# Performance work log

Measured on AMD Instinct MI355X. Metric: run time of the kernel, lower is better.

Reference implementation:

```python
import jax, jax.numpy as jnp
import numpy as np

N = 100000   # nodes
H = 96       # hidden_dim
A = 32       # attn_dim
De = 16      # edge_embeddings_dim
E = 500000   # edges per edge type
NEG_SLOPE = 0.01  # torch F.leaky_relu default


def setup_inputs() -> dict:
    key = jax.random.key(0)
    ks = jax.random.split(key, 24)
    nrm = lambda k, shape, s=1.0: jax.random.normal(k, shape, dtype=jnp.float32) * s
    idx = lambda k: jax.random.randint(k, (E,), 0, N, dtype=jnp.int32)
    Din = 2 * H + De
    return {
        'h': nrm(ks[0], (N, H)),
        'src0': idx(ks[1]), 'dst0': idx(ks[2]),
        'src1': idx(ks[3]), 'dst1': idx(ks[4]),
        'src2': idx(ks[5]), 'dst2': idx(ks[6]),
        'Wm0': nrm(ks[7], (Din, H), Din ** -0.5), 'bm0': jnp.zeros((H,), jnp.float32), 'ef0': nrm(ks[8], (De,)),
        'Wm1': nrm(ks[9], (Din, H), Din ** -0.5), 'bm1': jnp.zeros((H,), jnp.float32), 'ef1': nrm(ks[10], (De,)),
        'Wm2': nrm(ks[11], (Din, H), Din ** -0.5), 'bm2': jnp.zeros((H,), jnp.float32), 'ef2': nrm(ks[12], (De,)),
        'Wn0': nrm(ks[13], (H, A), H ** -0.5), 'Wa0': nrm(ks[14], (2 * A, 1), (2 * A) ** -0.5),
        'Wn1': nrm(ks[15], (H, A), H ** -0.5), 'Wa1': nrm(ks[16], (2 * A, 1), (2 * A) ** -0.5),
        'Wu': nrm(ks[17], (4 * H, H), (4 * H) ** -0.5), 'bu': jnp.zeros((H,), jnp.float32),
    }


def _leaky(x):
    return jnp.where(x > 0, x, NEG_SLOPE * x)


def _edge_msg(h, src, dst, Wm, bm, ef):
    # cat(src_h, dst_h, edge_feature) -> Linear  (dropout p=0, eval mode)
    x = jnp.concatenate([h[src], h[dst], jnp.broadcast_to(ef, (src.shape[0], ef.shape[0]))], axis=-1)
    return x @ Wm + bm  # [E, H]


def _mean_agg(m, dst):
    # fn.mean('m','msg'): per-destination mean over incoming edges
    s = jax.ops.segment_sum(m, dst, num_segments=N)
    c = jax.ops.segment_sum(jnp.ones((m.shape[0],), m.dtype), dst, num_segments=N)
    return s / jnp.maximum(c, 1.0)[:, None]


def _attn_agg(scores, m, dst):
    # per-destination softmax over mailbox (variable-size), then weighted sum
    smax = jax.ops.segment_max(scores, dst, num_segments=N)
    ex = jnp.exp(scores - smax[dst])
    den = jax.ops.segment_sum(ex, dst, num_segments=N)
    num = jax.ops.segment_sum(ex[:, None] * m, dst, num_segments=N)
    return num / jnp.maximum(den, 1e-9)[:, None]


def reference(h, src0, dst0, src1, dst1, src2, dst2,
              Wm0, bm0, ef0, Wm1, bm1, ef1, Wm2, bm2, ef2,
              Wn0, Wa0, Wn1, Wa1, Wu, bu):
    # edge type 0: intra_diff (attention), type 1: inter_diff (attention), type 2: intra_lt (mean)
    m0 = _edge_msg(h, src0, dst0, Wm0, bm0, ef0)
    m1 = _edge_msg(h, src1, dst1, Wm1, bm1, ef1)
    m2 = _edge_msg(h, src2, dst2, Wm2, bm2, ef2)

    z0 = h @ Wn0  # [N, A]
    s0 = _leaky(jnp.concatenate([z0[src0], z0[dst0]], axis=-1) @ Wa0)[:, 0]  # [E]
    z1 = h @ Wn1
    s1 = _leaky(jnp.concatenate([z1[src1], z1[dst1]], axis=-1) @ Wa1)[:, 0]

    msg0 = _attn_agg(s0, m0, dst0)   # [N, H]
    msg1 = _attn_agg(s1, m1, dst1)
    msg2 = _mean_agg(m2, dst2)

    # cross_reducer='stack' then concat over edge-type dim -> [N, 3H]
    mcat = jnp.concatenate([msg0, msg1, msg2], axis=-1)
    # cell node update: Linear(cat(h, m)) + ReLU
    return jax.nn.relu(jnp.concatenate([h, mcat], axis=-1) @ Wu + bu)
```

## Files before the change

### kernel.cpp

```cpp
#include <hip/hip_runtime.h>
#include <hip/hip_bf16.h>
#include <cstdint>

#define NN 100000
#define HH 96
#define AD 32
#define DE 16
#define EE 500000
#define NEG 0.01f

#define GSH 10
#define GSZ 1024
#define KB 98
#define CH 4096
#define BPT 123

typedef __bf16 bf16x8 __attribute__((ext_vector_type(8)));
typedef float  f32x4  __attribute__((ext_vector_type(4)));

__device__ __forceinline__ unsigned short f2b(float x) {
    union { float f; unsigned int u; } v; v.f = x;
    unsigned int r = v.u + 0x7fffu + ((v.u >> 16) & 1u);
    return (unsigned short)(r >> 16);
}
__device__ __forceinline__ float b2f(unsigned short h) {
    union { unsigned int u; float f; } v; v.u = ((unsigned int)h) << 16;
    return v.f;
}

__global__ void prep_kernel(const float* Wm0, const float* bm0, const float* ef0,
                            const float* Wm1, const float* bm1, const float* ef1,
                            const float* Wm2, const float* bm2, const float* ef2,
                            const float* Wn0, const float* Wa0,
                            const float* Wn1, const float* Wa1,
                            const float* Wu,
                            float* cvec, float* wvec,
                            unsigned short* BfN, unsigned short* BfU) {
    const float* Wm[3] = {Wm0, Wm1, Wm2};
    const float* bm[3] = {bm0, bm1, bm2};
    const float* ef[3] = {ef0, ef1, ef2};
    const int total = 288 + 384 + 55296 + 36864;
    for (int i = blockIdx.x * blockDim.x + threadIdx.x; i < total;
         i += gridDim.x * blockDim.x) {
        if (i < 288) {
            int t = i / 96, j = i % 96;
            float s = bm[t][j];
            for (int k = 0; k < DE; ++k) s += ef[t][k] * Wm[t][(2 * HH + k) * HH + j];
            cvec[i] = s;
        } else if (i < 288 + 384) {
            int ii = i - 288;
            int kind = ii / 96, k = ii % 96;
            const float* Wn = (kind < 2) ? Wn0 : Wn1;
            const float* Wa = (kind < 2) ? Wa0 : Wa1;
            int off = (kind & 1) ? AD : 0;
            float s = 0.f;
            for (int a = 0; a < AD; ++a) s += Wn[k * AD + a] * Wa[off + a];
            wvec[ii] = s;
        } else if (i < 288 + 384 + 55296) {
            int ii = i - 672;
            int sec = ii / 9216; int rem = ii % 9216;
            int ksc = rem / 512; int lj = rem % 512;
            int ks = ksc / 6, c = ksc % 6;
            int lane = lj / 8, jj = lj % 8;
            int quad = lane / 16, m = lane % 16;
            int k = ks * 32 + quad * 8 + jj;
            int n = c * 16 + m;
            int mt = (sec < 3) ? sec : sec - 3;
            int rowoff = (sec < 3) ? 0 : HH;
            BfN[ii] = f2b(Wm[mt][(rowoff + k) * HH + n]);
        } else {
            int ii = i - (672 + 55296);
            int ksc = ii / 512; int lj = ii % 512;
            int ks = ksc / 6, c = ksc % 6;
            int lane = lj / 8, jj = lj % 8;
            int quad = lane / 16, m = lane % 16;
            int k = ks * 32 + quad * 8 + jj;
            int n = c * 16 + m;
            BfU[ii] = f2b(Wu[k * HH + n]);
        }
    }
}

__global__ void cast_uv_kernel(const float* __restrict__ h, const float* __restrict__ wvec,
                               unsigned short* __restrict__ hb, float* __restrict__ uv) {
    int lane = threadIdx.x & 31;
    int node = (blockIdx.x * blockDim.x + threadIdx.x) >> 5;
    if (node >= NN) return;
    float h0 = h[node * HH + lane];
    float h1 = h[node * HH + 32 + lane];
    float h2 = h[node * HH + 64 + lane];
    hb[node * HH + lane] = f2b(h0);
    hb[node * HH + 32 + lane] = f2b(h1);
    hb[node * HH + 64 + lane] = f2b(h2);
    float acc[4];
#pragma unroll
    for (int q = 0; q < 4; ++q)
        acc[q] = h0 * wvec[q * 96 + lane] + h1 * wvec[q * 96 + 32 + lane] +
                 h2 * wvec[q * 96 + 64 + lane];
#pragma unroll
    for (int d = 16; d >= 1; d >>= 1)
#pragma unroll
        for (int q = 0; q < 4; ++q) acc[q] += __shfl_down(acc[q], d, 32);
    if (lane == 0) {
#pragma unroll
        for (int q = 0; q < 4; ++q) uv[q * NN + node] = acc[q];
    }
}

__global__ void zero_kernel(float4* __restrict__ p, int n4) {
    for (int i = blockIdx.x * blockDim.x + threadIdx.x; i < n4;
         i += gridDim.x * blockDim.x)
        p[i] = make_float4(0.f, 0.f, 0.f, 0.f);
}

__global__ void bucket_hist(const int* __restrict__ d0, const int* __restrict__ d1,
                            const int* __restrict__ d2, int* __restrict__ bCnt) {
    __shared__ int hist[3 * KB];
    int t = threadIdx.x;
    for (int j = t; j < 3 * KB; j += 256) hist[j] = 0;
    __syncthreads();
    const int total = 3 * EE;
    for (int i = blockIdx.x * blockDim.x + t; i < total; i += gridDim.x * blockDim.x) {
        int ty = i / EE, e = i - ty * EE;
        const int* d = (ty == 0) ? d0 : (ty == 1) ? d1 : d2;
        atomicAdd(&hist[ty * KB + (d[e] >> GSH)], 1);
    }
    __syncthreads();
    for (int j = t; j < 3 * KB; j += 256)
        if (hist[j]) atomicAdd(&bCnt[j], hist[j]);
}

__global__ void bucket_scan(const int* __restrict__ bCnt, int* __restrict__ bBase,
                            int* __restrict__ gCursor, int* __restrict__ rs) {
    __shared__ int hist[3 * KB];
    int t = threadIdx.x;
    if (t < 3 * KB) hist[t] = bCnt[t];
    __syncthreads();
    if (t < 3) {
        int run = 0;
        for (int b = 0; b < KB; ++b) {
            bBase[t * (KB + 1) + b] = run;
            gCursor[t * KB + b] = run;
            run += hist[t * KB + b];
        }
        bBase[t * (KB + 1) + KB] = run;
        rs[(size_t)t * (NN + 1) + NN] = run;
    }
}

__global__ __launch_bounds__(256) void bucket_scatter(
    const int* __restrict__ s0, const int* __restrict__ d0,
    const int* __restrict__ s1, const int* __restrict__ d1,
    const int* __restrict__ s2, const int* __restrict__ d2,
    int* __restrict__ gCursor, unsigned int* __restrict__ binned) {
    __shared__ unsigned int recs[CH];
    __shared__ unsigned short rnk[CH];
    __shared__ unsigned char bkt[CH];
    __shared__ int cnt[KB];
    __shared__ int gpos[KB];
    int t = threadIdx.x;
    int type = blockIdx.x / BPT;
    int chunk = (blockIdx.x % BPT) * CH;
    const int* src = (type == 0) ? s0 : (type == 1) ? s1 : s2;
    const int* dst = (type == 0) ? d0 : (type == 1) ? d1 : d2;
    if (t < KB) cnt[t] = 0;
    __syncthreads();
#pragma unroll
    for (int k = 0; k < CH / 256; ++k) {
        int idx = k * 256 + t;
        int e = chunk + idx;
        if (e < EE) {
            int s = src[e], d = dst[e];
            int b = d >> GSH;
            recs[idx] = ((unsigned int)s << GSH) | (unsigned int)(d & (GSZ - 1));
            bkt[idx] = (unsigned char)b;
            rnk[idx] = (unsigned short)atomicAdd(&cnt[b], 1);
        } else {
            bkt[idx] = 0xFF;
        }
    }
    __syncthreads();
    if (t < KB) {
        int c = cnt[t];
        gpos[t] = (c > 0) ? atomicAdd(&gCursor[type * KB + t], c) : 0;
    }
    __syncthreads();
    unsigned int* bout = binned + (size_t)type * EE;
#pragma unroll
    for (int k = 0; k < CH / 256; ++k) {
        int idx = k * 256 + t;
        unsigned char b = bkt[idx];
        if (b != 0xFF) bout[gpos[b] + rnk[idx]] = recs[idx];
    }
}

__global__ __launch_bounds__(256) void bucket_sort(
    const unsigned int* __restrict__ binned, const int* __restrict__ bBase,
    int* __restrict__ rs, int* __restrict__ sorted) {
    __shared__ int cnt[GSZ];
    __shared__ int tsum[256];
    int t = threadIdx.x;
    int type = blockIdx.x / KB;
    int b = blockIdx.x % KB;
    int nodeBase = b * GSZ;
    int eb = bBase[type * (KB + 1) + b];
    int en = bBase[type * (KB + 1) + b + 1];
    int n = en - eb;
    const unsigned int* bin = binned + (size_t)type * EE + eb;
#pragma unroll
    for (int k = 0; k < GSZ / 256; ++k) cnt[k * 256 + t] = 0;
    __syncthreads();
    for (int i = t; i < n; i += 256) atomicAdd(&cnt[bin[i] & (GSZ - 1)], 1);
    __syncthreads();
    int v[4], s = 0;
#pragma unroll
    for (int k = 0; k < 4; ++k) { v[k] = cnt[t * 4 + k]; s += v[k]; }
    tsum[t] = s;
    __syncthreads();
    for (int off = 1; off < 256; off <<= 1) {
        int add = (t >= off) ? tsum[t - off] : 0;
        __syncthreads();
        tsum[t] += add;
        __syncthreads();
    }
    int run = tsum[t] - s;
    int offk[4];
#pragma unroll
    for (int k = 0; k < 4; ++k) { offk[k] = run; run += v[k]; }
    int* rsrow = rs + (size_t)type * (NN + 1) + nodeBase;
#pragma unroll
    for (int k = 0; k < 4; ++k) {
        int node = t * 4 + k;
        if (nodeBase + node < NN) rsrow[node] = eb + offk[k];
    }
    __syncthreads();
#pragma unroll
    for (int k = 0; k < 4; ++k) cnt[t * 4 + k] = offk[k];
    __syncthreads();
    int* so = sorted + (size_t)type * EE + eb;
    for (int i = t; i < n; i += 256) {
        unsigned int r = bin[i];
        int dl = r & (GSZ - 1);
        int p = atomicAdd(&cnt[dl], 1);
        so[p] = (int)(r >> GSH);
    }
}

__global__ void aggregate_kernel(const int* __restrict__ rsAll, const int* __restrict__ sortedAll,
                                 const float* __restrict__ uv,
                                 const unsigned short* __restrict__ hb,
                                 unsigned short* __restrict__ hagg,
                                 float* __restrict__ den) {
    const size_t NH = (size_t)NN * HH;
    int lane = threadIdx.x & 31;
    int node = (blockIdx.x * blockDim.x + threadIdx.x) >> 5;
    if (node >= NN) return;
    int t = blockIdx.y;
    int is_attn = (t < 2);
    const int* rs = rsAll + (size_t)t * (NN + 1);
    const int* sorted = sortedAll + (size_t)t * EE;
    const float* u = uv + 2 * t * NN;

    int beg = rs[node], end = rs[node + 1];
    float a0 = 0.f, a1 = 0.f, a2 = 0.f, dn = 0.f;
    float vd = is_attn ? uv[(2 * t + 1) * NN + node] : 0.f;
    for (int base = beg; base < end; base += 32) {
        int batch = end - base;
        if (batch > 32) batch = 32;
        int li = lane < batch ? lane : batch - 1;
        int myS = sorted[base + li];
#pragma unroll 1
        for (int j = 0; j < batch; j += 8) {
            int rem = batch - j;
            int sI[8];
            float wv[8];
#pragma unroll
            for (int k = 0; k < 8; ++k) sI[k] = __shfl(myS, (k < rem ? j + k : j), 32);
            if (is_attn) {
#pragma unroll
                for (int k = 0; k < 8; ++k) {
                    float c = u[sI[k]] + vd;
                    c = c > 0.f ? c : NEG * c;
                    wv[k] = __expf(c);
                }
            } else {
#pragma unroll
                for (int k = 0; k < 8; ++k) wv[k] = 1.f;
            }
#pragma unroll
            for (int k = 0; k < 8; ++k) if (k >= rem) wv[k] = 0.f;
            float x0[8], x1[8], x2[8];
#pragma unroll
            for (int k = 0; k < 8; ++k) {
                const unsigned short* pr = hb + (size_t)sI[k] * HH;
                x0[k] = b2f(pr[lane]);
                x1[k] = b2f(pr[lane + 32]);
                x2[k] = b2f(pr[lane + 64]);
            }
#pragma unroll
            for (int k = 0; k < 8; ++k) {
                dn += wv[k];
                a0 += wv[k] * x0[k];
                a1 += wv[k] * x1[k];
                a2 += wv[k] * x2[k];
            }
        }
    }
    float r0 = 0.f, r1 = 0.f, r2 = 0.f;
    if (dn > 0.f) {
        float inv = 1.f / dn;
        r0 = a0 * inv; r1 = a1 * inv; r2 = a2 * inv;
    }
    unsigned short* mr = hagg + (size_t)t * NH + (size_t)node * HH;
    mr[lane] = f2b(r0);
    mr[lane + 32] = f2b(r1);
    mr[lane + 64] = f2b(r2);
    if (lane == 0) den[(size_t)t * NN + node] = dn;
}

__global__ __launch_bounds__(256) void msg_gemm_kernel(const unsigned short* __restrict__ hagg,
                                                       const unsigned short* __restrict__ hb,
                                                       const unsigned short* __restrict__ BfN,
                                                       const float* __restrict__ den,
                                                       const float* __restrict__ cvec,
                                                       unsigned short* __restrict__ msgb) {
    const size_t NH = (size_t)NN * HH;
    int wave = threadIdx.x >> 6;
    int lane = threadIdx.x & 63;
    int quad = lane >> 4, m = lane & 15;
    int blk = blockIdx.x * 4 + wave;
    if (blk >= NN / 16) return;
    int t = blockIdx.y;
    int r0 = blk * 16;
    const unsigned short* ha = hagg + (size_t)t * NH;
    f32x4 acc[6] = {};
#pragma unroll
    for (int ks = 0; ks < 6; ++ks) {
        const unsigned short* ap =
            (ks < 3) ? ha + (size_t)(r0 + m) * HH + ks * 32 + quad * 8
                     : hb + (size_t)(r0 + m) * HH + (ks - 3) * 32 + quad * 8;
        int sec = (ks < 3) ? t : t + 3;
        int kk = (ks < 3) ? ks : ks - 3;
        bf16x8 af = *(const bf16x8*)ap;
#pragma unroll
        for (int c = 0; c < 6; ++c) {
            bf16x8 bfv = *(const bf16x8*)(BfN + (((sec * 3 + kk) * 6 + c) << 9) + lane * 8);
            acc[c] = __builtin_amdgcn_mfma_f32_16x16x32_bf16(af, bfv, acc[c], 0, 0, 0);
        }
    }
    float dn[4];
#pragma unroll
    for (int r = 0; r < 4; ++r) dn[r] = den[(size_t)t * NN + r0 + quad * 4 + r];
#pragma unroll
    for (int c = 0; c < 6; ++c) {
        float cv = cvec[t * 96 + c * 16 + m];
#pragma unroll
        for (int r = 0; r < 4; ++r) {
            int row = r0 + quad * 4 + r;
            float val = (dn[r] > 0.f) ? (acc[c][r] + cv) : 0.f;
            msgb[(size_t)row * 288 + t * 96 + c * 16 + m] = f2b(val);
        }
    }
}

__global__ __launch_bounds__(256) void update_gemm_kernel(const unsigned short* __restrict__ hb,
                                                          const unsigned short* __restrict__ msgb,
                                                          const unsigned short* __restrict__ BfU,
                                                          const float* __restrict__ bu,
                                                          float* __restrict__ out) {
    int wave = threadIdx.x >> 6;
    int lane = threadIdx.x & 63;
    int quad = lane >> 4, m = lane & 15;
    int blk = blockIdx.x * 4 + wave;
    if (blk >= NN / 16) return;
    int r0 = blk * 16;
    f32x4 acc[6] = {};
#pragma unroll
    for (int ks = 0; ks < 12; ++ks) {
        const unsigned short* ap =
            (ks < 3) ? hb + (size_t)(r0 + m) * HH + ks * 32 + quad * 8
                     : msgb + (size_t)(r0 + m) * 288 + (ks - 3) * 32 + quad * 8;
        bf16x8 af = *(const bf16x8*)ap;
#pragma unroll
        for (int c = 0; c < 6; ++c) {
            bf16x8 bfv = *(const bf16x8*)(BfU + ((ks * 6 + c) << 9) + lane * 8);
            acc[c] = __builtin_amdgcn_mfma_f32_16x16x32_bf16(af, bfv, acc[c], 0, 0, 0);
        }
    }
#pragma unroll
    for (int c = 0; c < 6; ++c) {
        float b = bu[c * 16 + m];
#pragma unroll
        for (int r = 0; r < 4; ++r) {
            int row = r0 + quad * 4 + r;
            float v2 = acc[c][r] + b;
            out[(size_t)row * HH + c * 16 + m] = v2 > 0.f ? v2 : 0.f;
        }
    }
}

extern "C" void kernel_launch(void* const* d_in, const int* in_sizes, int n_in,
                              void* d_out, int out_size, void* d_ws, size_t ws_size,
                              hipStream_t stream) {
    (void)in_sizes; (void)n_in; (void)out_size;
    const float* h   = (const float*)d_in[0];
    const int* srcs[3] = {(const int*)d_in[1], (const int*)d_in[3], (const int*)d_in[5]};
    const int* dsts[3] = {(const int*)d_in[2], (const int*)d_in[4], (const int*)d_in[6]};
    const float* Wm0 = (const float*)d_in[7];
    const float* bm0 = (const float*)d_in[8];
    const float* ef0 = (const float*)d_in[9];
    const float* Wm1 = (const float*)d_in[10];
    const float* bm1 = (const float*)d_in[11];
    const float* ef1 = (const float*)d_in[12];
    const float* Wm2 = (const float*)d_in[13];
    const float* bm2 = (const float*)d_in[14];
    const float* ef2 = (const float*)d_in[15];
    const float* Wn0 = (const float*)d_in[16];
    const float* Wa0 = (const float*)d_in[17];
    const float* Wn1 = (const float*)d_in[18];
    const float* Wa1 = (const float*)d_in[19];
    const float* Wu  = (const float*)d_in[20];
    const float* bu  = (const float*)d_in[21];
    float* out = (float*)d_out;

    const size_t NEED = 150591104;
    if (ws_size < NEED) return;
    char* w = (char*)d_ws;
    unsigned short* msgb    = (unsigned short*)(w + 0);
    unsigned short* hb      = (unsigned short*)(w + 57600000);
    unsigned short* hagg    = (unsigned short*)(w + 76800000);
    float*          den     = (float*)(w + 134400000);
    float*          uv      = (float*)(w + 135600000);
    float*          cvec    = (float*)(w + 137200000);
    float*          wvec    = (float*)(w + 137201280);
    unsigned short* BfN     = (unsigned short*)(w + 137202816);
    unsigned short* BfU     = (unsigned short*)(w + 137313408);
    int*            bBase   = (int*)(w + 137387136);
    int*            gCursor = (int*)(w + 137388416);
    int*            bCnt    = (int*)(w + 137389696);
    int*            rs      = (int*)(w + 137390976);
    int*            sorted  = (int*)(w + 138591104);
    unsigned int*   binned  = (unsigned int*)(w + 144591104);

    prep_kernel<<<128, 256, 0, stream>>>(Wm0, bm0, ef0, Wm1, bm1, ef1, Wm2, bm2, ef2,
                                         Wn0, Wa0, Wn1, Wa1, Wu, cvec, wvec, BfN, BfU);
    cast_uv_kernel<<<12500, 256, 0, stream>>>(h, wvec, hb, uv);

    zero_kernel<<<1, 256, 0, stream>>>((float4*)bCnt, 80);
    bucket_hist<<<512, 256, 0, stream>>>(dsts[0], dsts[1], dsts[2], bCnt);
    bucket_scan<<<1, 384, 0, stream>>>(bCnt, bBase, gCursor, rs);
    bucket_scatter<<<3 * BPT, 256, 0, stream>>>(srcs[0], dsts[0], srcs[1], dsts[1],
                                                srcs[2], dsts[2], gCursor, binned);
    bucket_sort<<<3 * KB, 256, 0, stream>>>(binned, bBase, rs, sorted);

    aggregate_kernel<<<dim3(12500, 3), 256, 0, stream>>>(rs, sorted, uv, hb, hagg, den);
    msg_gemm_kernel<<<dim3(1563, 3), 256, 0, stream>>>(hagg, hb, BfN, den, cvec, msgb);
    update_gemm_kernel<<<1563, 256, 0, stream>>>(hb, msgb, BfU, bu, out);
}
```

Baseline: 331.5 us.

## Fuse message and update GEMMs via LDS; precompute attention weights in sort

The separate message GEMM and update GEMM are merged into one kernel. Each wave computes its three per-type message tiles, stages them in shared memory and feeds them straight into the update GEMM, so the large bf16 message buffer is never written to or read back from global memory. The attention exp weights are now computed once per edge inside bucket_sort and stored beside the sorted source indices. The aggregate kernel then reads and shuffles the weight instead of gathering u and taking an exp per edge. This adds a 2 MB-per-type weight array and more LDS per block in the fused kernel, which may lower occupancy.

```diff
diff --git a/kernel.cpp b/kernel.cpp
--- a/kernel.cpp
+++ b/kernel.cpp
@@ -196,7 +196,8 @@
 
 __global__ __launch_bounds__(256) void bucket_sort(
     const unsigned int* __restrict__ binned, const int* __restrict__ bBase,
-    int* __restrict__ rs, int* __restrict__ sorted) {
+    const float* __restrict__ uv,
+    int* __restrict__ rs, int* __restrict__ sorted, float* __restrict__ expw) {
     __shared__ int cnt[GSZ];
     __shared__ int tsum[256];
     int t = threadIdx.x;
@@ -238,16 +239,27 @@
     for (int k = 0; k < 4; ++k) cnt[t * 4 + k] = offk[k];
     __syncthreads();
     int* so = sorted + (size_t)type * EE + eb;
+    float* ew = expw + (size_t)type * EE + eb;
+    const float* u = uv + 2 * type * NN;
+    const float* vv = uv + (2 * type + 1) * NN;
     for (int i = t; i < n; i += 256) {
         unsigned int r = bin[i];
         int dl = r & (GSZ - 1);
         int p = atomicAdd(&cnt[dl], 1);
-        so[p] = (int)(r >> GSH);
+        int srcn = (int)(r >> GSH);
+        so[p] = srcn;
+        float wgt = 1.f;
+        if (type < 2) {
+            float sc = u[srcn] + vv[nodeBase + dl];
+            sc = sc > 0.f ? sc : NEG * sc;
+            wgt = __expf(sc);
+        }
+        ew[p] = wgt;
     }
 }
 
 __global__ void aggregate_kernel(const int* __restrict__ rsAll, const int* __restrict__ sortedAll,
-                                 const float* __restrict__ uv,
+                                 const float* __restrict__ expwAll,
                                  const unsigned short* __restrict__ hb,
                                  unsigned short* __restrict__ hagg,
                                  float* __restrict__ den) {
@@ -256,36 +268,28 @@
     int node = (blockIdx.x * blockDim.x + threadIdx.x) >> 5;
     if (node >= NN) return;
     int t = blockIdx.y;
-    int is_attn = (t < 2);
     const int* rs = rsAll + (size_t)t * (NN + 1);
     const int* sorted = sortedAll + (size_t)t * EE;
-    const float* u = uv + 2 * t * NN;
+    const float* expw = expwAll + (size_t)t * EE;
 
     int beg = rs[node], end = rs[node + 1];
     float a0 = 0.f, a1 = 0.f, a2 = 0.f, dn = 0.f;
-    float vd = is_attn ? uv[(2 * t + 1) * NN + node] : 0.f;
     for (int base = beg; base < end; base += 32) {
         int batch = end - base;
         if (batch > 32) batch = 32;
         int li = lane < batch ? lane : batch - 1;
         int myS = sorted[base + li];
+        float myW = expw[base + li];
 #pragma unroll 1
         for (int j = 0; j < batch; j += 8) {
             int rem = batch - j;
             int sI[8];
             float wv[8];
 #pragma unroll
-            for (int k = 0; k < 8; ++k) sI[k] = __shfl(myS, (k < rem ? j + k : j), 32);
-            if (is_attn) {
-#pragma unroll
-                for (int k = 0; k < 8; ++k) {
-                    float c = u[sI[k]] + vd;
-                    c = c > 0.f ? c : NEG * c;
-                    wv[k] = __expf(c);
-                }
-            } else {
-#pragma unroll
-                for (int k = 0; k < 8; ++k) wv[k] = 1.f;
+            for (int k = 0; k < 8; ++k) {
+                int jj = (k < rem ? j + k : j);
+                sI[k] = __shfl(myS, jj, 32);
+                wv[k] = __shfl(myW, jj, 32);
             }
 #pragma unroll
             for (int k = 0; k < 8; ++k) if (k >= rem) wv[k] = 0.f;
@@ -318,83 +322,82 @@
     if (lane == 0) den[(size_t)t * NN + node] = dn;
 }
 
-__global__ __launch_bounds__(256) void msg_gemm_kernel(const unsigned short* __restrict__ hagg,
-                                                       const unsigned short* __restrict__ hb,
-                                                       const unsigned short* __restrict__ BfN,
-                                                       const float* __restrict__ den,
-                                                       const float* __restrict__ cvec,
-                                                       unsigned short* __restrict__ msgb) {
+#define MSP 296
+__global__ __launch_bounds__(256) void fused_update_kernel(
+    const unsigned short* __restrict__ hagg, const unsigned short* __restrict__ hb,
+    const unsigned short* __restrict__ BfN, const unsigned short* __restrict__ BfU,
+    const float* __restrict__ den, const float* __restrict__ cvec,
+    const float* __restrict__ bu, float* __restrict__ out) {
+    __shared__ unsigned short msgt[4][16][MSP];
     const size_t NH = (size_t)NN * HH;
     int wave = threadIdx.x >> 6;
     int lane = threadIdx.x & 63;
     int quad = lane >> 4, m = lane & 15;
     int blk = blockIdx.x * 4 + wave;
-    if (blk >= NN / 16) return;
-    int t = blockIdx.y;
+    bool active = (blk < NN / 16);
     int r0 = blk * 16;
-    const unsigned short* ha = hagg + (size_t)t * NH;
-    f32x4 acc[6] = {};
-#pragma unroll
-    for (int ks = 0; ks < 6; ++ks) {
-        const unsigned short* ap =
-            (ks < 3) ? ha + (size_t)(r0 + m) * HH + ks * 32 + quad * 8
-                     : hb + (size_t)(r0 + m) * HH + (ks - 3) * 32 + quad * 8;
-        int sec = (ks < 3) ? t : t + 3;
-        int kk = (ks < 3) ? ks : ks - 3;
-        bf16x8 af = *(const bf16x8*)ap;
+    bf16x8 hfrag[3];
+    if (active) {
+        const unsigned short* hrow = hb + (size_t)(r0 + m) * HH + quad * 8;
+#pragma unroll
+        for (int ks = 0; ks < 3; ++ks) hfrag[ks] = *(const bf16x8*)(hrow + ks * 32);
+#pragma unroll
+        for (int t = 0; t < 3; ++t) {
+            f32x4 acc[6] = {};
+            const unsigned short* harow = hagg + (size_t)t * NH + (size_t)(r0 + m) * HH + quad * 8;
+#pragma unroll
+            for (int ks = 0; ks < 3; ++ks) {
+                bf16x8 af = *(const bf16x8*)(harow + ks * 32);
+#pragma unroll
+                for (int c = 0; c < 6; ++c) {
+                    bf16x8 bfv = *(const bf16x8*)(BfN + (((t * 3 + ks) * 6 + c) << 9) + lane * 8);
+                    acc[c] = __builtin_amdgcn_mfma_f32_16x16x32_bf16(af, bfv, acc[c], 0, 0, 0);
+                }
+            }
+#pragma unroll
+            for (int ks = 0; ks < 3; ++ks) {
+#pragma unroll
+                for (int c = 0; c < 6; ++c) {
+                    bf16x8 bfv = *(const bf16x8*)(BfN + ((((t + 3) * 3 + ks) * 6 + c) << 9) + lane * 8);
+                    acc[c] = __builtin_amdgcn_mfma_f32_16x16x32_bf16(hfrag[ks], bfv, acc[c], 0, 0, 0);
+                }
+            }
+            float dnv[4];
+#pragma unroll
+            for (int r = 0; r < 4; ++r) dnv[r] = den[(size_t)t * NN + r0 + quad * 4 + r];
+#pragma unroll
+            for (int c = 0; c < 6; ++c) {
+                float cv = cvec[t * 96 + c * 16 + m];
+#pragma unroll
+                for (int r = 0; r < 4; ++r) {
+                    float val = (dnv[r] > 0.f) ? (acc[c][r] + cv) : 0.f;
+                    msgt[wave][quad * 4 + r][t * 96 + c * 16 + m] = f2b(val);
+                }
+            }
+        }
+    }
+    __syncthreads();
+    if (active) {
+        f32x4 acc2[6] = {};
+#pragma unroll
+        for (int ks = 0; ks < 12; ++ks) {
+            bf16x8 af = (ks < 3) ? hfrag[ks]
+                                 : *(const bf16x8*)&msgt[wave][m][(ks - 3) * 32 + quad * 8];
+#pragma unroll
+            for (int c = 0; c < 6; ++c) {
+                bf16x8 bfv = *(const bf16x8*)(BfU + ((ks * 6 + c) << 9) + lane * 8);
+                acc2[c] = __builtin_amdgcn_mfma_f32_16x16x32_bf16(af, bfv, acc2[c], 0, 0, 0);
+            }
+        }
 #pragma unroll
         for (int c = 0; c < 6; ++c) {
-            bf16x8 bfv = *(const bf16x8*)(BfN + (((sec * 3 + kk) * 6 + c) << 9) + lane * 8);
-            acc[c] = __builtin_amdgcn_mfma_f32_16x16x32_bf16(af, bfv, acc[c], 0, 0, 0);
-        }
-    }
-    float dn[4];
-#pragma unroll
-    for (int r = 0; r < 4; ++r) dn[r] = den[(size_t)t * NN + r0 + quad * 4 + r];
-#pragma unroll
-    for (int c = 0; c < 6; ++c) {
-        float cv = cvec[t * 96 + c * 16 + m];
-#pragma unroll
-        for (int r = 0; r < 4; ++r) {
-            int row = r0 + quad * 4 + r;
-            float val = (dn[r] > 0.f) ? (acc[c][r] + cv) : 0.f;
-            msgb[(size_t)row * 288 + t * 96 + c * 16 + m] = f2b(val);
-        }
-    }
-}
-
-__global__ __launch_bounds__(256) void update_gemm_kernel(const unsigned short* __restrict__ hb,
-                                                          const unsigned short* __restrict__ msgb,
-                                                          const unsigned short* __restrict__ BfU,
-                                                          const float* __restrict__ bu,
-                                                          float* __restrict__ out) {
-    int wave = threadIdx.x >> 6;
-    int lane = threadIdx.x & 63;
-    int quad = lane >> 4, m = lane & 15;
-    int blk = blockIdx.x * 4 + wave;
-    if (blk >= NN / 16) return;
-    int r0 = blk * 16;
-    f32x4 acc[6] = {};
-#pragma unroll
-    for (int ks = 0; ks < 12; ++ks) {
-        const unsigned short* ap =
-            (ks < 3) ? hb + (size_t)(r0 + m) * HH + ks * 32 + quad * 8
-                     : msgb + (size_t)(r0 + m) * 288 + (ks - 3) * 32 + quad * 8;
-        bf16x8 af = *(const bf16x8*)ap;
-#pragma unroll
-        for (int c = 0; c < 6; ++c) {
-            bf16x8 bfv = *(const bf16x8*)(BfU + ((ks * 6 + c) << 9) + lane * 8);
-            acc[c] = __builtin_amdgcn_mfma_f32_16x16x32_bf16(af, bfv, acc[c], 0, 0, 0);
-        }
-    }
-#pragma unroll
-    for (int c = 0; c < 6; ++c) {
-        float b = bu[c * 16 + m];
-#pragma unroll
-        for (int r = 0; r < 4; ++r) {
-            int row = r0 + quad * 4 + r;
-            float v2 = acc[c][r] + b;
-            out[(size_t)row * HH + c * 16 + m] = v2 > 0.f ? v2 : 0.f;
+            float b = bu[c * 16 + m];
+#pragma unroll
+            for (int r = 0; r < 4; ++r) {
+                int row = r0 + quad * 4 + r;
+                float v2 = acc2[c][r] + b;
+                out[(size_t)row * HH + c * 16 + m] = v2 > 0.f ? v2 : 0.f;
+            }
         }
     }
 }
@@ -423,24 +426,24 @@
     const float* bu  = (const float*)d_in[21];
     float* out = (float*)d_out;
 
-    const size_t NEED = 150591104;
+    const size_t NEED = 98991104;
     if (ws_size < NEED) return;
     char* w = (char*)d_ws;
-    unsigned short* msgb    = (unsigned short*)(w + 0);
-    unsigned short* hb      = (unsigned short*)(w + 57600000);
-    unsigned short* hagg    = (unsigned short*)(w + 76800000);
-    float*          den     = (float*)(w + 134400000);
-    float*          uv      = (float*)(w + 135600000);
-    float*          cvec    = (float*)(w + 137200000);
-    float*          wvec    = (float*)(w + 137201280);
-    unsigned short* BfN     = (unsigned short*)(w + 137202816);
-    unsigned short* BfU     = (unsigned short*)(w + 137313408);
-    int*            bBase   = (int*)(w + 137387136);
-    int*            gCursor = (int*)(w + 137388416);
-    int*            bCnt    = (int*)(w + 137389696);
-    int*            rs      = (int*)(w + 137390976);
-    int*            sorted  = (int*)(w + 138591104);
-    unsigned int*   binned  = (unsigned int*)(w + 144591104);
+    unsigned short* hb      = (unsigned short*)(w + 0);
+    unsigned short* hagg    = (unsigned short*)(w + 19200000);
+    float*          den     = (float*)(w + 76800000);
+    float*          uv      = (float*)(w + 78000000);
+    float*          cvec    = (float*)(w + 79600000);
+    float*          wvec    = (float*)(w + 79601280);
+    unsigned short* BfN     = (unsigned short*)(w + 79602816);
+    unsigned short* BfU     = (unsigned short*)(w + 79713408);
+    int*            bBase   = (int*)(w + 79787136);
+    int*            gCursor = (int*)(w + 79788416);
+    int*            bCnt    = (int*)(w + 79789696);
+    int*            rs      = (int*)(w + 79790976);
+    int*            sorted  = (int*)(w + 80991104);
+    unsigned int*   binned  = (unsigned int*)(w + 86991104);
+    float*          expw    = (float*)(w + 92991104);
 
     prep_kernel<<<128, 256, 0, stream>>>(Wm0, bm0, ef0, Wm1, bm1, ef1, Wm2, bm2, ef2,
                                          Wn0, Wa0, Wn1, Wa1, Wu, cvec, wvec, BfN, BfU);
@@ -451,9 +454,8 @@
     bucket_scan<<<1, 384, 0, stream>>>(bCnt, bBase, gCursor, rs);
     bucket_scatter<<<3 * BPT, 256, 0, stream>>>(srcs[0], dsts[0], srcs[1], dsts[1],
                                                 srcs[2], dsts[2], gCursor, binned);
-    bucket_sort<<<3 * KB, 256, 0, stream>>>(binned, bBase, rs, sorted);
-
-    aggregate_kernel<<<dim3(12500, 3), 256, 0, stream>>>(rs, sorted, uv, hb, hagg, den);
-    msg_gemm_kernel<<<dim3(1563, 3), 256, 0, stream>>>(hagg, hb, BfN, den, cvec, msgb);
-    update_gemm_kernel<<<1563, 256, 0, stream>>>(hb, msgb, BfU, bu, out);
-}
+    bucket_sort<<<3 * KB, 256, 0, stream>>>(binned, bBase, uv, rs, sorted, expw);
+
+    aggregate_kernel<<<dim3(12500, 3), 256, 0, stream>>>(rs, sorted, expw, hb, hagg, den);
+    fused_update_kernel<<<1563, 256, 0, stream>>>(hagg, hb, BfN, BfU, den, cvec, bu, out);
+}
```

Measured after the change: 346.7 us. +4.6%, slower.
